# Optimization experiments

Hardware: AMD Instinct MI355X
Metric: run time of the kernel (lower is better)

Reference implementation:

```python
import jax, jax.numpy as jnp
import numpy as np

B, CIN, COUT, H, W = 4, 256, 128, 64, 64

def conv1x1(x, w, b):
    # x: [B,C,H,W], w: [O,C], b: [O]
    return jnp.einsum('bchw,oc->bohw', x, w) + b[None, :, None, None]

def setup_inputs() -> dict:
    key = jax.random.key(0)
    ks = jax.random.split(key, 9)
    s_in = 1.0 / np.sqrt(CIN)
    s_out = 1.0 / np.sqrt(COUT)
    return {
        'x': jax.random.normal(ks[0], (B, CIN, H, W), dtype=jnp.float32),
        'w_theta': jax.random.normal(ks[1], (COUT, CIN), dtype=jnp.float32) * s_in,
        'b_theta': jax.random.normal(ks[2], (COUT,), dtype=jnp.float32) * s_in,
        'w_phi': jax.random.normal(ks[3], (COUT, CIN), dtype=jnp.float32) * s_in,
        'b_phi': jax.random.normal(ks[4], (COUT,), dtype=jnp.float32) * s_in,
        'w_g': jax.random.normal(ks[5], (COUT, CIN), dtype=jnp.float32) * s_in,
        'b_g': jax.random.normal(ks[6], (COUT,), dtype=jnp.float32) * s_in,
        'w_W': jax.random.normal(ks[7], (CIN, COUT), dtype=jnp.float32) * s_out,
        'b_W': jax.random.normal(ks[8], (CIN,), dtype=jnp.float32) * s_out,
    }

def reference(x, w_theta, b_theta, w_phi, b_phi, w_g, b_g, w_W, b_W):
    b, c, h, w = x.shape
    n = h * w
    co = w_theta.shape[0]
    theta_x = conv1x1(x, w_theta, b_theta).reshape(b, co, n).transpose(0, 2, 1)  # [B,N,Co]
    phi_x = conv1x1(x, w_phi, b_phi).reshape(b, co, n)                            # [B,Co,N]
    g_x = conv1x1(x, w_g, b_g).reshape(b, co, n).transpose(0, 2, 1)               # [B,N,Co]
    scores = jnp.einsum('bnc,bcm->bnm', theta_x, phi_x)                           # [B,N,N]
    attn = jax.nn.softmax(scores, axis=-1)
    y = jnp.einsum('bnm,bmc->bnc', attn, g_x)                                     # [B,N,Co]
    y = y.transpose(0, 2, 1).reshape(b, co, h, w)
    z = conv1x1(y, w_W, b_W) + x
    return z
```

## Files before the change

kernel.cpp:

```cpp
#include <hip/hip_runtime.h>

#define B_    4
#define C_    256
#define O_    128
#define N_    4096
#define THW   256
#define TILES 64

typedef __attribute__((ext_vector_type(8))) _Float16 f16x8;
typedef __attribute__((ext_vector_type(4))) float    f32x4;

struct __align__(8) us4 { unsigned short x, y, z, w; };

__device__ __forceinline__ float bf2f(unsigned short u) {
    unsigned v = ((unsigned)u) << 16;
    union { unsigned u; float f; } c; c.u = v; return c.f;
}
__device__ __forceinline__ unsigned short f2bf(float f) {
    union { float f; unsigned u; } c; c.f = f;
    unsigned r = c.u + 0x7fffu + ((c.u >> 16) & 1u);
    return (unsigned short)(r >> 16);
}
__device__ __forceinline__ unsigned short f2h(float f) {
    _Float16 h = (_Float16)f;
    union { _Float16 h; unsigned short s; } c; c.h = h; return c.s;
}
__device__ __forceinline__ float h2f(unsigned short s) {
    union { unsigned short s; _Float16 h; } c; c.s = s; return (float)c.h;
}

__device__ __forceinline__ void load4f(const void* base, size_t idx, int isf32, float o[4]) {
    if (isf32) {
        float4 v = *(const float4*)((const float*)base + idx);
        o[0] = v.x; o[1] = v.y; o[2] = v.z; o[3] = v.w;
    } else {
        us4 v = *(const us4*)((const unsigned short*)base + idx);
        o[0] = bf2f(v.x); o[1] = bf2f(v.y); o[2] = bf2f(v.z); o[3] = bf2f(v.w);
    }
}
__device__ __forceinline__ float load1f(const void* base, size_t idx, int isf32) {
    return isf32 ? ((const float*)base)[idx] : bf2f(((const unsigned short*)base)[idx]);
}

__global__ __launch_bounds__(256) void detect_kernel(
    const unsigned short* __restrict__ xu, int* __restrict__ flag)
{
    __shared__ int cnt;
    if (threadIdx.x == 0) cnt = 0;
    __syncthreads();
    int local = 0;
    for (int i = threadIdx.x; i < 4096; i += 256) {
        unsigned short u = xu[2 * i];
        int e = (u >> 7) & 0xFF;
        if (e == 0xFF || e >= 0x90 || (e > 0 && e <= 0x60)) local++;
    }
    atomicAdd(&cnt, local);
    __syncthreads();
    if (threadIdx.x == 0) *flag = (cnt > 1024) ? 1 : 0;
}

__global__ __launch_bounds__(256) void qkv_kernel(
    const void* __restrict__ x,
    const void* __restrict__ wt, const void* __restrict__ wp,
    const void* __restrict__ wg,
    const void* __restrict__ bt, const void* __restrict__ bp,
    const void* __restrict__ bg,
    const int*  __restrict__ flag,
    unsigned short* __restrict__ thph,
    unsigned short* __restrict__ gT)
{
    const int isf32 = *flag;
    const int jsel = blockIdx.y;
    const void* w  = jsel == 0 ? wt : (jsel == 1 ? wp : wg);
    const void* bi = jsel == 0 ? bt : (jsel == 1 ? bp : bg);
    const int b  = blockIdx.z;
    const int n0 = blockIdx.x * 64;
    const int tid  = threadIdx.x;
    const int wv   = tid >> 6, lane = tid & 63;
    const int quad = lane >> 4, l16 = lane & 15;

    __shared__ alignas(16) unsigned short smem[64 * 72 + 128 * 72];
    unsigned short (*As)[72] = (unsigned short(*)[72])smem;
    unsigned short (*Bs)[72] = (unsigned short(*)[72])(smem + 64 * 72);

    f32x4 acc[8];
    for (int i = 0; i < 8; i++) acc[i] = (f32x4)0.f;

    for (int kc = 0; kc < C_; kc += 64) {
        __syncthreads();
        for (int it = 0; it < 4; it++) {
            int l = it * 256 + tid;
            int c = l >> 4;
            int ng = l & 15;
            float v[4];
            load4f(x, (size_t)(b * C_ + kc + c) * N_ + n0 + ng * 4, isf32, v);
            int g = c >> 3, cl = c & 7;
            int swz = ((g ^ (ng & 7)) << 3) + cl;
            As[ng * 4 + 0][swz] = f2h(v[0]);
            As[ng * 4 + 1][swz] = f2h(v[1]);
            As[ng * 4 + 2][swz] = f2h(v[2]);
            As[ng * 4 + 3][swz] = f2h(v[3]);
        }
        for (int it = 0; it < 8; it++) {
            int l = it * 256 + tid;
            int j = l >> 4;
            int cg = l & 15;
            float v[4];
            load4f(w, (size_t)j * C_ + kc + cg * 4, isf32, v);
            us4 pk;
            pk.x = f2h(v[0]); pk.y = f2h(v[1]); pk.z = f2h(v[2]); pk.w = f2h(v[3]);
            *(us4*)&Bs[j][cg * 4] = pk;
        }
        __syncthreads();
        for (int s = 0; s < 2; s++) {
            int row = wv * 16 + l16;
            int g2 = ((s * 4 + quad) ^ ((row >> 2) & 7)) << 3;
            f16x8 a = *(const f16x8*)&As[row][g2];
            for (int jt = 0; jt < 8; jt++) {
                f16x8 bb = *(const f16x8*)&Bs[jt * 16 + l16][s * 32 + quad * 8];
                acc[jt] = __builtin_amdgcn_mfma_f32_16x16x32_f16(a, bb, acc[jt], 0, 0, 0);
            }
        }
    }

    if (jsel < 2) {
        const float scale = (jsel == 0) ? 1.44269504f : 1.0f;
        for (int jt = 0; jt < 8; jt++) {
            int j = jt * 16 + l16;
            float bias = load1f(bi, j, isf32);
            for (int r = 0; r < 4; r++) {
                int n = n0 + wv * 16 + quad * 4 + r;
                thph[(size_t)(b * N_ + n) * THW + jsel * O_ + j] = f2h((acc[jt][r] + bias) * scale);
            }
        }
    } else {
        unsigned short (*T)[68] = (unsigned short(*)[68])smem;
        __syncthreads();
        for (int jt = 0; jt < 8; jt++) {
            int j = jt * 16 + l16;
            float bias = load1f(bi, j, isf32);
            for (int r = 0; r < 4; r++) {
                int nl = wv * 16 + quad * 4 + r;
                T[j][nl] = f2h(acc[jt][r] + bias);
            }
        }
        __syncthreads();
        for (int it = 0; it < 8; it++) {
            int l = it * 256 + tid;
            int j = l >> 4;
            int ng = l & 15;
            *(us4*)(gT + ((size_t)(b * O_ + j)) * N_ + n0 + ng * 4) = *(const us4*)&T[j][ng * 4];
        }
    }
}

__global__ __launch_bounds__(256, 2) void attn_partial(
    const unsigned short* __restrict__ thph,
    const unsigned short* __restrict__ gT,
    unsigned short* __restrict__ partO,
    float* __restrict__ pm,
    float* __restrict__ pl,
    int S)
{
    const int b    = blockIdx.z;
    const int s_id = blockIdx.y;
    const int n0   = blockIdx.x * 128;
    const int tid  = threadIdx.x;
    const int wv   = tid >> 6, lane = tid & 63;
    const int quad = lane >> 4, l16 = lane & 15;

    const int t0 = (TILES * s_id) / S;
    const int t1 = (TILES * (s_id + 1)) / S;

    __shared__ alignas(16) unsigned short Ks[64][136];
    __shared__ alignas(16) unsigned short Gs[128][72];
    __shared__ alignas(16) unsigned short Ps[4][32][72];

    const int wq0 = n0 + wv * 32;

    f16x8 qf[2][4];
    #pragma unroll
    for (int qg = 0; qg < 2; qg++) {
        const unsigned short* qp = thph + (size_t)(b * N_ + wq0 + qg * 16 + l16) * THW;
        #pragma unroll
        for (int s = 0; s < 4; s++)
            qf[qg][s] = *(const f16x8*)(qp + s * 32 + quad * 8);
    }

    f32x4 oacc[2][8];
    #pragma unroll
    for (int qg = 0; qg < 2; qg++)
        #pragma unroll
        for (int i = 0; i < 8; i++) oacc[qg][i] = (f32x4)0.f;
    float mst[2] = { -INFINITY, -INFINITY };
    float lst[2] = { 0.f, 0.f };

    const int krow = tid >> 4, kog = tid & 15;
    const int grow = tid >> 3, gng = tid & 7;
    const unsigned short* kb_g = thph + (size_t)(b * N_ + krow) * THW + O_ + kog * 8;
    const unsigned short* gb_g = gT + ((size_t)(b * O_ + grow)) * N_ + gng * 8;

    f16x8 kreg[4], greg[4];
    auto prefetch = [&](int mt) {
        int m0 = mt * 64;
        #pragma unroll
        for (int it = 0; it < 4; it++)
            kreg[it] = *(const f16x8*)(kb_g + (size_t)(m0 + it * 16) * THW);
        #pragma unroll
        for (int it = 0; it < 4; it++)
            greg[it] = *(const f16x8*)(gb_g + m0 + (size_t)it * 32 * N_);
    };
    prefetch(t0);

    for (int mt = t0; mt < t1; mt++) {
        __syncthreads();
        #pragma unroll
        for (int it = 0; it < 4; it++)
            *(f16x8*)&Ks[krow + it * 16][kog * 8] = kreg[it];
        #pragma unroll
        for (int it = 0; it < 4; it++)
            *(f16x8*)&Gs[grow + it * 32][gng * 8] = greg[it];
        __syncthreads();
        if (mt + 1 < t1) prefetch(mt + 1);

        f32x4 sacc[2][4];
        #pragma unroll
        for (int qg = 0; qg < 2; qg++)
            #pragma unroll
            for (int kt = 0; kt < 4; kt++) sacc[qg][kt] = (f32x4)0.f;
        __builtin_amdgcn_s_setprio(1);
        #pragma unroll
        for (int s = 0; s < 4; s++) {
            #pragma unroll
            for (int kt = 0; kt < 4; kt++) {
                f16x8 kb = *(const f16x8*)&Ks[kt * 16 + l16][s * 32 + quad * 8];
                sacc[0][kt] = __builtin_amdgcn_mfma_f32_16x16x32_f16(kb, qf[0][s], sacc[0][kt], 0, 0, 0);
                sacc[1][kt] = __builtin_amdgcn_mfma_f32_16x16x32_f16(kb, qf[1][s], sacc[1][kt], 0, 0, 0);
            }
        }
        __builtin_amdgcn_s_setprio(0);

        #pragma unroll
        for (int qg = 0; qg < 2; qg++) {
            float rm = fmaxf(
                fmaxf(fmaxf(fmaxf(sacc[qg][0][0], sacc[qg][0][1]), fmaxf(sacc[qg][0][2], sacc[qg][0][3])),
                      fmaxf(fmaxf(sacc[qg][1][0], sacc[qg][1][1]), fmaxf(sacc[qg][1][2], sacc[qg][1][3]))),
                fmaxf(fmaxf(fmaxf(sacc[qg][2][0], sacc[qg][2][1]), fmaxf(sacc[qg][2][2], sacc[qg][2][3])),
                      fmaxf(fmaxf(sacc[qg][3][0], sacc[qg][3][1]), fmaxf(sacc[qg][3][2], sacc[qg][3][3]))));
            rm = fmaxf(rm, __shfl_xor(rm, 16));
            rm = fmaxf(rm, __shfl_xor(rm, 32));

            if (__any(rm > mst[qg] + 8.0f)) {
                float mnew  = fmaxf(mst[qg], rm);
                float alpha = exp2f(mst[qg] - mnew);
                mst[qg] = mnew;
                lst[qg] *= alpha;
                #pragma unroll
                for (int jt = 0; jt < 8; jt++) oacc[qg][jt] *= alpha;
            }
            const float m = mst[qg];

            float rs = 0.f;
            unsigned short* prow = &Ps[wv][qg * 16 + l16][quad * 4];
            #pragma unroll
            for (int kt = 0; kt < 4; kt++) {
                float p0 = exp2f(sacc[qg][kt][0] - m);
                float p1 = exp2f(sacc[qg][kt][1] - m);
                float p2 = exp2f(sacc[qg][kt][2] - m);
                float p3 = exp2f(sacc[qg][kt][3] - m);
                rs += (p0 + p1) + (p2 + p3);
                us4 pk;
                pk.x = f2h(p0); pk.y = f2h(p1); pk.z = f2h(p2); pk.w = f2h(p3);
                *(us4*)(prow + kt * 16) = pk;
            }
            rs += __shfl_xor(rs, 16);
            rs += __shfl_xor(rs, 32);
            lst[qg] += rs;
        }

        __builtin_amdgcn_s_setprio(1);
        #pragma unroll
        for (int s = 0; s < 2; s++) {
            f16x8 pb0 = *(const f16x8*)&Ps[wv][l16][s * 32 + quad * 8];
            f16x8 pb1 = *(const f16x8*)&Ps[wv][16 + l16][s * 32 + quad * 8];
            #pragma unroll
            for (int jt = 0; jt < 8; jt++) {
                f16x8 ga = *(const f16x8*)&Gs[jt * 16 + l16][s * 32 + quad * 8];
                oacc[0][jt] = __builtin_amdgcn_mfma_f32_16x16x32_f16(ga, pb0, oacc[0][jt], 0, 0, 0);
                oacc[1][jt] = __builtin_amdgcn_mfma_f32_16x16x32_f16(ga, pb1, oacc[1][jt], 0, 0, 0);
            }
        }
        __builtin_amdgcn_s_setprio(0);
    }

    #pragma unroll
    for (int qg = 0; qg < 2; qg++) {
        int n = wq0 + qg * 16 + l16;
        size_t rowb = ((size_t)(s_id * B_ + b) * N_ + n) * O_;
        #pragma unroll
        for (int jt = 0; jt < 8; jt++) {
            us4 v;
            v.x = f2h(oacc[qg][jt][0]);
            v.y = f2h(oacc[qg][jt][1]);
            v.z = f2h(oacc[qg][jt][2]);
            v.w = f2h(oacc[qg][jt][3]);
            *(us4*)(partO + rowb + jt * 16 + quad * 4) = v;
        }
        if (quad == 0) {
            pm[(size_t)(s_id * B_ + b) * N_ + n] = mst[qg];
            pl[(size_t)(s_id * B_ + b) * N_ + n] = lst[qg];
        }
    }
}

__global__ __launch_bounds__(256) void merge_kernel(
    const unsigned short* __restrict__ partO,
    const float* __restrict__ pm, const float* __restrict__ pl,
    unsigned short* __restrict__ y,
    int S)
{
    int idx = blockIdx.x * 256 + threadIdx.x;
    int bn  = idx >> 5;
    int og  = idx & 31;
    const int BN = B_ * N_;

    float M = -INFINITY;
    for (int s = 0; s < S; s++) M = fmaxf(M, pm[(size_t)s * BN + bn]);

    float L = 0.f;
    float a0 = 0.f, a1 = 0.f, a2 = 0.f, a3 = 0.f;
    for (int s = 0; s < S; s++) {
        float ws = exp2f(pm[(size_t)s * BN + bn] - M);
        L += ws * pl[(size_t)s * BN + bn];
        us4 v = *(const us4*)(partO + ((size_t)s * BN + bn) * O_ + og * 4);
        a0 += h2f(v.x) * ws;
        a1 += h2f(v.y) * ws;
        a2 += h2f(v.z) * ws;
        a3 += h2f(v.w) * ws;
    }
    float inv = 1.0f / L;

    us4 r;
    r.x = f2h(a0 * inv); r.y = f2h(a1 * inv);
    r.z = f2h(a2 * inv); r.w = f2h(a3 * inv);
    *(us4*)(y + (size_t)bn * O_ + og * 4) = r;
}

__global__ __launch_bounds__(256) void out_kernel(
    const unsigned short* __restrict__ y,
    const void* __restrict__ wW,
    const void* __restrict__ bW,
    const void* __restrict__ x,
    const int*  __restrict__ flag,
    void* __restrict__ z)
{
    const int isf32 = *flag;
    const int b  = blockIdx.z;
    const int c0 = blockIdx.y * 64;
    const int n0 = blockIdx.x * 128;
    const int tid  = threadIdx.x;
    const int wv   = tid >> 6, lane = tid & 63;
    const int quad = lane >> 4, l16 = lane & 15;

    __shared__ alignas(16) unsigned short Ys[128][136];
    __shared__ alignas(16) unsigned short Ws[64][136];

    for (int it = 0; it < 16; it++) {
        int l = it * 256 + tid;
        int nn = l >> 5;
        int og = l & 31;
        us4 v = *(const us4*)(y + (size_t)(b * N_ + n0 + nn) * O_ + og * 4);
        *(us4*)&Ys[nn][og * 4] = v;
    }
    for (int it = 0; it < 8; it++) {
        int l = it * 256 + tid;
        int cc = l >> 5;
        int og = l & 31;
        float v[4];
        load4f(wW, (size_t)(c0 + cc) * O_ + og * 4, isf32, v);
        us4 pk;
        pk.x = f2h(v[0]); pk.y = f2h(v[1]); pk.z = f2h(v[2]); pk.w = f2h(v[3]);
        *(us4*)&Ws[cc][og * 4] = pk;
    }
    __syncthreads();

    f32x4 acc[8];
    for (int i = 0; i < 8; i++) acc[i] = (f32x4)0.f;
    for (int s = 0; s < 4; s++) {
        f16x8 a = *(const f16x8*)&Ws[wv * 16 + l16][s * 32 + quad * 8];
        for (int nt = 0; nt < 8; nt++) {
            f16x8 bb = *(const f16x8*)&Ys[nt * 16 + l16][s * 32 + quad * 8];
            acc[nt] = __builtin_amdgcn_mfma_f32_16x16x32_f16(a, bb, acc[nt], 0, 0, 0);
        }
    }
    for (int r = 0; r < 4; r++) {
        int c = c0 + wv * 16 + quad * 4 + r;
        float bias = load1f(bW, c, isf32);
        for (int nt = 0; nt < 8; nt++) {
            int n = n0 + nt * 16 + l16;
            size_t idx = (size_t)(b * C_ + c) * N_ + n;
            float zv = acc[nt][r] + bias + load1f(x, idx, isf32);
            if (isf32) ((float*)z)[idx] = zv;
            else       ((unsigned short*)z)[idx] = f2bf(zv);
        }
    }
}

extern "C" void kernel_launch(void* const* d_in, const int* in_sizes, int n_in,
                              void* d_out, int out_size, void* d_ws, size_t ws_size,
                              hipStream_t stream) {
    const void* x  = d_in[0];
    const void* wt = d_in[1];
    const void* bt = d_in[2];
    const void* wp = d_in[3];
    const void* bp = d_in[4];
    const void* wg = d_in[5];
    const void* bg = d_in[6];
    const void* wW = d_in[7];
    const void* bW = d_in[8];

    const size_t base = 64 + 8388608  + 4194304 ;
    const size_t per_split = 4194304  + 131072 ;
    int S = 6;
    while (S > 1 && base + (size_t)S * per_split > ws_size) S--;

    char* p = (char*)d_ws;
    int* flag = (int*)p;                    p += 64;
    unsigned short* thph = (unsigned short*)p;  p += 8388608;
    unsigned short* gT   = (unsigned short*)p;  p += 4194304;
    unsigned short* partO = (unsigned short*)p; p += (size_t)S * 4194304;
    float* pm = (float*)p;                  p += (size_t)S * 65536;
    float* pl = (float*)p;
    unsigned short* y = gT;

    detect_kernel<<<1, 256, 0, stream>>>((const unsigned short*)x, flag);

    dim3 g1(N_ / 64, 3, B_);
    qkv_kernel<<<g1, 256, 0, stream>>>(x, wt, wp, wg, bt, bp, bg, flag, thph, gT);

    dim3 g2(N_ / 128, S, B_);
    attn_partial<<<g2, 256, 0, stream>>>(thph, gT, partO, pm, pl, S);

    merge_kernel<<<(B_ * N_ * 32) / 256, 256, 0, stream>>>(partO, pm, pl, y, S);

    dim3 g3(N_ / 128, C_ / 64, B_);
    out_kernel<<<g3, 256, 0, stream>>>(y, wW, bW, x, flag, d_out);
}
```

Before: 191.4 us.

## Vectorize epilogues via swapped MFMA operands, always-rescale softmax, fewer KV splits

The QKV projection swaps its MFMA operands so each lane holds four consecutive output channels, which lets the theta/phi stores and bias loads become packed 4-wide accesses. The output projection is retiled so each lane holds four consecutive pixels, giving vectorized float4/us4 loads of x and stores of z. In attention the lazy max-rescale threshold and the setprio hints are removed, so the accumulator is rescaled every tile. The split count drops from 6 to 4, which cuts partial-result traffic but also reduces the number of parallel blocks.

```diff
diff --git a/kernel.cpp b/kernel.cpp
--- a/kernel.cpp
+++ b/kernel.cpp
@@ -118,30 +118,34 @@
             f16x8 a = *(const f16x8*)&As[row][g2];
             for (int jt = 0; jt < 8; jt++) {
                 f16x8 bb = *(const f16x8*)&Bs[jt * 16 + l16][s * 32 + quad * 8];
-                acc[jt] = __builtin_amdgcn_mfma_f32_16x16x32_f16(a, bb, acc[jt], 0, 0, 0);
+                acc[jt] = __builtin_amdgcn_mfma_f32_16x16x32_f16(bb, a, acc[jt], 0, 0, 0);
             }
         }
     }
 
     if (jsel < 2) {
         const float scale = (jsel == 0) ? 1.44269504f : 1.0f;
+        int n = n0 + wv * 16 + l16;
+        unsigned short* orow = thph + (size_t)(b * N_ + n) * THW + jsel * O_;
         for (int jt = 0; jt < 8; jt++) {
-            int j = jt * 16 + l16;
-            float bias = load1f(bi, j, isf32);
-            for (int r = 0; r < 4; r++) {
-                int n = n0 + wv * 16 + quad * 4 + r;
-                thph[(size_t)(b * N_ + n) * THW + jsel * O_ + j] = f2h((acc[jt][r] + bias) * scale);
-            }
+            float bv[4];
+            load4f(bi, jt * 16 + quad * 4, isf32, bv);
+            us4 pk;
+            pk.x = f2h((acc[jt][0] + bv[0]) * scale);
+            pk.y = f2h((acc[jt][1] + bv[1]) * scale);
+            pk.z = f2h((acc[jt][2] + bv[2]) * scale);
+            pk.w = f2h((acc[jt][3] + bv[3]) * scale);
+            *(us4*)(orow + jt * 16 + quad * 4) = pk;
         }
     } else {
         unsigned short (*T)[68] = (unsigned short(*)[68])smem;
         __syncthreads();
         for (int jt = 0; jt < 8; jt++) {
-            int j = jt * 16 + l16;
-            float bias = load1f(bi, j, isf32);
+            float bv[4];
+            load4f(bi, jt * 16 + quad * 4, isf32, bv);
             for (int r = 0; r < 4; r++) {
-                int nl = wv * 16 + quad * 4 + r;
-                T[j][nl] = f2h(acc[jt][r] + bias);
+                int j = jt * 16 + quad * 4 + r;
+                T[j][wv * 16 + l16] = f2h(acc[jt][r] + bv[r]);
             }
         }
         __syncthreads();
@@ -228,7 +232,6 @@
         for (int qg = 0; qg < 2; qg++)
             #pragma unroll
             for (int kt = 0; kt < 4; kt++) sacc[qg][kt] = (f32x4)0.f;
-        __builtin_amdgcn_s_setprio(1);
         #pragma unroll
         for (int s = 0; s < 4; s++) {
             #pragma unroll
@@ -238,7 +241,6 @@
                 sacc[1][kt] = __builtin_amdgcn_mfma_f32_16x16x32_f16(kb, qf[1][s], sacc[1][kt], 0, 0, 0);
             }
         }
-        __builtin_amdgcn_s_setprio(0);
 
         #pragma unroll
         for (int qg = 0; qg < 2; qg++) {
@@ -250,24 +252,18 @@
             rm = fmaxf(rm, __shfl_xor(rm, 16));
             rm = fmaxf(rm, __shfl_xor(rm, 32));
 
-            if (__any(rm > mst[qg] + 8.0f)) {
-                float mnew  = fmaxf(mst[qg], rm);
-                float alpha = exp2f(mst[qg] - mnew);
-                mst[qg] = mnew;
-                lst[qg] *= alpha;
-                #pragma unroll
-                for (int jt = 0; jt < 8; jt++) oacc[qg][jt] *= alpha;
-            }
-            const float m = mst[qg];
+            float mnew  = fmaxf(mst[qg], rm);
+            float alpha = exp2f(mst[qg] - mnew);
+            mst[qg] = mnew;
 
             float rs = 0.f;
             unsigned short* prow = &Ps[wv][qg * 16 + l16][quad * 4];
             #pragma unroll
             for (int kt = 0; kt < 4; kt++) {
-                float p0 = exp2f(sacc[qg][kt][0] - m);
-                float p1 = exp2f(sacc[qg][kt][1] - m);
-                float p2 = exp2f(sacc[qg][kt][2] - m);
-                float p3 = exp2f(sacc[qg][kt][3] - m);
+                float p0 = exp2f(sacc[qg][kt][0] - mnew);
+                float p1 = exp2f(sacc[qg][kt][1] - mnew);
+                float p2 = exp2f(sacc[qg][kt][2] - mnew);
+                float p3 = exp2f(sacc[qg][kt][3] - mnew);
                 rs += (p0 + p1) + (p2 + p3);
                 us4 pk;
                 pk.x = f2h(p0); pk.y = f2h(p1); pk.z = f2h(p2); pk.w = f2h(p3);
@@ -275,10 +271,12 @@
             }
             rs += __shfl_xor(rs, 16);
             rs += __shfl_xor(rs, 32);
-            lst[qg] += rs;
-        }
-
-        __builtin_amdgcn_s_setprio(1);
+            lst[qg] = lst[qg] * alpha + rs;
+
+            #pragma unroll
+            for (int jt = 0; jt < 8; jt++) oacc[qg][jt] *= alpha;
+        }
+
         #pragma unroll
         for (int s = 0; s < 2; s++) {
             f16x8 pb0 = *(const f16x8*)&Ps[wv][l16][s * 32 + quad * 8];
@@ -290,7 +288,6 @@
                 oacc[1][jt] = __builtin_amdgcn_mfma_f32_16x16x32_f16(ga, pb1, oacc[1][jt], 0, 0, 0);
             }
         }
-        __builtin_amdgcn_s_setprio(0);
     }
 
     #pragma unroll
@@ -384,24 +381,47 @@
     }
     __syncthreads();
 
-    f32x4 acc[8];
-    for (int i = 0; i < 8; i++) acc[i] = (f32x4)0.f;
+    f32x4 acc[2][4];
+    for (int nt = 0; nt < 2; nt++)
+        for (int ct = 0; ct < 4; ct++) acc[nt][ct] = (f32x4)0.f;
     for (int s = 0; s < 4; s++) {
-        f16x8 a = *(const f16x8*)&Ws[wv * 16 + l16][s * 32 + quad * 8];
-        for (int nt = 0; nt < 8; nt++) {
-            f16x8 bb = *(const f16x8*)&Ys[nt * 16 + l16][s * 32 + quad * 8];
-            acc[nt] = __builtin_amdgcn_mfma_f32_16x16x32_f16(a, bb, acc[nt], 0, 0, 0);
-        }
-    }
-    for (int r = 0; r < 4; r++) {
-        int c = c0 + wv * 16 + quad * 4 + r;
+        f16x8 af[2];
+        #pragma unroll
+        for (int nt = 0; nt < 2; nt++)
+            af[nt] = *(const f16x8*)&Ys[wv * 32 + nt * 16 + l16][s * 32 + quad * 8];
+        #pragma unroll
+        for (int ct = 0; ct < 4; ct++) {
+            f16x8 wf = *(const f16x8*)&Ws[ct * 16 + l16][s * 32 + quad * 8];
+            acc[0][ct] = __builtin_amdgcn_mfma_f32_16x16x32_f16(af[0], wf, acc[0][ct], 0, 0, 0);
+            acc[1][ct] = __builtin_amdgcn_mfma_f32_16x16x32_f16(af[1], wf, acc[1][ct], 0, 0, 0);
+        }
+    }
+
+    #pragma unroll
+    for (int ct = 0; ct < 4; ct++) {
+        int c = c0 + ct * 16 + l16;
         float bias = load1f(bW, c, isf32);
-        for (int nt = 0; nt < 8; nt++) {
-            int n = n0 + nt * 16 + l16;
+        #pragma unroll
+        for (int nt = 0; nt < 2; nt++) {
+            int n = n0 + wv * 32 + nt * 16 + quad * 4;
             size_t idx = (size_t)(b * C_ + c) * N_ + n;
-            float zv = acc[nt][r] + bias + load1f(x, idx, isf32);
-            if (isf32) ((float*)z)[idx] = zv;
-            else       ((unsigned short*)z)[idx] = f2bf(zv);
+            if (isf32) {
+                float4 xv = *(const float4*)((const float*)x + idx);
+                float4 zv;
+                zv.x = acc[nt][ct][0] + bias + xv.x;
+                zv.y = acc[nt][ct][1] + bias + xv.y;
+                zv.z = acc[nt][ct][2] + bias + xv.z;
+                zv.w = acc[nt][ct][3] + bias + xv.w;
+                *(float4*)((float*)z + idx) = zv;
+            } else {
+                us4 xv = *(const us4*)((const unsigned short*)x + idx);
+                us4 zv;
+                zv.x = f2bf(acc[nt][ct][0] + bias + bf2f(xv.x));
+                zv.y = f2bf(acc[nt][ct][1] + bias + bf2f(xv.y));
+                zv.z = f2bf(acc[nt][ct][2] + bias + bf2f(xv.z));
+                zv.w = f2bf(acc[nt][ct][3] + bias + bf2f(xv.w));
+                *(us4*)((unsigned short*)z + idx) = zv;
+            }
         }
     }
 }
@@ -421,7 +441,7 @@
 
     const size_t base = 64 + 8388608  + 4194304 ;
     const size_t per_split = 4194304  + 131072 ;
-    int S = 6;
+    int S = 4;
     while (S > 1 && base + (size_t)S * per_split > ws_size) S--;
 
     char* p = (char*)d_ws;
```

Measured after the change: 184.2 us (median of 2 runs). 3.8% less time.
